# Kernel tuning notes

Hardware: AMD Instinct MI355X
Metric: run time of the kernel (lower is better)

## Reference

```python
import jax, jax.numpy as jnp
import numpy as np

ALPHA = 0.2  # LeakyReLU slope in GAT
OUT_SLOPE = 0.01  # default nn.LeakyyReLU slope for self.out
B, E, IN_DIM, HID, HEADS = 4, 2048, 32, 18, 3
DH = HID // HEADS  # per-head out dim = 6


def _leaky(x, slope):
    return jnp.where(x > 0, x, slope * x)


def _gat_head(x, adj, W, a):
    # x: [B,E,in], W: [in,dh], a: [2*dh,1]
    h = jnp.einsum('bei,id->bed', x, W)                      # [B,E,dh]
    d = h.shape[-1]
    # score[b,i,j] = leakyrelu(a . concat(h_i, h_j)) = leakyrelu(h_i.a1 + h_j.a2)
    e1 = jnp.einsum('bed,d->be', h, a[:d, 0])
    e2 = jnp.einsum('bed,d->be', h, a[d:, 0])
    score = _leaky(e1[:, :, None] + e2[:, None, :], ALPHA)   # [B,E,E]
    scores = jnp.where(adj == 1.0, score, 0.0)
    logits = jnp.where(adj > 0.0, scores, -30.0)
    att = jax.nn.softmax(logits, axis=2)                     # softmax over j
    # h_prime[b,j,d] = sum_i att[b,i,j] * h[b,i,d]  (torch sums over dim=1)
    h_prime = jnp.einsum('bij,bid->bjd', att, h)
    return jax.nn.elu(h_prime)  # concat=True -> elu


def _gat_multihead(x, adj, Ws, As):
    # Ws: [H,in,dh], As: [H,2*dh,1]
    outs = jax.vmap(lambda W, a: _gat_head(x, adj, W, a))(Ws, As)  # [H,B,E,dh]
    H, b, e, d = outs.shape
    return jnp.moveaxis(outs, 0, 2).reshape(b, e, H * d)  # concat heads last-dim


def _gcn(x, adj2d, W, b):
    return adj2d @ (x @ W) + b


def setup_inputs() -> dict:
    key = jax.random.key(0)
    ks = jax.random.split(key, 16)
    node_input = jax.random.normal(ks[0], (B, E, IN_DIM), jnp.float32)
    uv_filed = jax.random.normal(ks[1], (B, E, IN_DIM), jnp.float32)
    adj = jax.random.randint(ks[2], (B, E, E), 0, 2).astype(jnp.float32)
    s = 0.1
    Wt1 = jax.random.normal(ks[3], (HEADS, IN_DIM, DH), jnp.float32) * s
    at1 = jax.random.normal(ks[4], (HEADS, 2 * DH, 1), jnp.float32) * s
    Wt2 = jax.random.normal(ks[5], (HEADS, IN_DIM, DH), jnp.float32) * s
    at2 = jax.random.normal(ks[6], (HEADS, 2 * DH, 1), jnp.float32) * s
    Wg1 = jax.random.normal(ks[7], (HID, 16), jnp.float32) * s
    bg1 = jnp.zeros((16,), jnp.float32)
    Wg2 = jax.random.normal(ks[8], (16, 2), jnp.float32) * s
    bg2 = jnp.zeros((2,), jnp.float32)
    Wo1 = jax.random.normal(ks[9], (HID, 16), jnp.float32) * s
    bo1 = jnp.zeros((16,), jnp.float32)
    Wo2 = jax.random.normal(ks[10], (16, 2), jnp.float32) * s
    bo2 = jnp.zeros((2,), jnp.float32)
    return dict(node_input=node_input, uv_filed=uv_filed, adj=adj,
                Wt1=Wt1, at1=at1, Wt2=Wt2, at2=at2,
                Wg1=Wg1, bg1=bg1, Wg2=Wg2, bg2=bg2,
                Wo1=Wo1, bo1=bo1, Wo2=Wo2, bo2=bo2)


def reference(node_input, uv_filed, adj, Wt1, at1, Wt2, at2,
              Wg1, bg1, Wg2, bg2, Wo1, bo1, Wo2, bo2):
    h = _gat_multihead(node_input, adj, Wt1, at1)  # [B,E,18]
    o = _gat_multihead(uv_filed, adj, Wt2, at2)    # [B,E,18]
    a0 = adj[0]
    Y = jax.nn.relu(_gcn(h[0], a0, Wg1, bg1))
    O = jax.nn.relu(_gcn(o[0], a0, Wo1, bo1))
    Y = _gcn(Y, a0, Wg2, bg2)
    O = _gcn(O, a0, Wo2, bo2)
    return (jax.nn.log_softmax(Y, axis=1), _leaky(O, OUT_SLOPE))
```

## Files before the change

### kernel.cpp

```cpp
#include <hip/hip_runtime.h>
#include <hip/hip_bf16.h>


__global__ __launch_bounds__(256) void k01(
    const float* __restrict__ adj0, unsigned int* __restrict__ bm,
    const float* __restrict__ node, const float* __restrict__ uv,
    const float* __restrict__ Wt1, const float* __restrict__ at1,
    const float* __restrict__ Wt2, const float* __restrict__ at2,
    float* __restrict__ hcol, float4* __restrict__ pk1q, float* __restrict__ pack2) {
  int b = blockIdx.x;
  if (b < 512) {
    int lane = threadIdx.x & 63, w = threadIdx.x >> 6;
    int row = b * 4 + w;
    const float* arow = adj0 + (size_t)row * 2048;
#pragma unroll 4
    for (int it = 0; it < 32; ++it) {
      float v = arow[it * 64 + lane];
      unsigned long long mask = __ballot(v == 1.0f);
      if (lane == 0) bm[row * 64 + it * 2] = (unsigned int)mask;
      else if (lane == 32) bm[row * 64 + it * 2 + 1] = (unsigned int)(mask >> 32);
    }
    return;
  }
  __shared__ float sW[192];
  __shared__ float sA[12];
  int fb = b - 512;
  int g = fb / 24;
  int h = (fb / 8) % 3;
  int e = (fb % 8) * 256 + threadIdx.x;
  const float* W = (g ? Wt2 : Wt1) + h * 192;
  const float* A = (g ? at2 : at1) + h * 12;
  const float* x = (g ? uv : node) + e * 32;
  if (threadIdx.x < 192) sW[threadIdx.x] = W[threadIdx.x];
  if (threadIdx.x < 12) sA[threadIdx.x] = A[threadIdx.x];
  __syncthreads();
  float xv[32];
#pragma unroll
  for (int i = 0; i < 32; ++i) xv[i] = x[i];
  float hv[6];
#pragma unroll
  for (int d = 0; d < 6; ++d) hv[d] = 0.f;
#pragma unroll
  for (int i = 0; i < 32; ++i)
#pragma unroll
    for (int d = 0; d < 6; ++d) hv[d] += xv[i] * sW[i * 6 + d];
  float e1 = 0.f, e2 = 0.f;
#pragma unroll
  for (int d = 0; d < 6; ++d) {
    e1 += hv[d] * sA[d];
    e2 += hv[d] * sA[6 + d];
  }
  int c = g * 3 + h;
#pragma unroll
  for (int d = 0; d < 6; ++d) hcol[(c * 6 + d) * 2048 + e] = hv[d];
  pk1q[c * 2048 + e] = make_float4(e1, __expf(e1), __expf(0.2f * e1), 0.f);
  pack2[c * 2048 + e] = e2;
  pack2[(6 + c) * 2048 + e] = __expf(e2);
  pack2[(12 + c) * 2048 + e] = __expf(0.2f * e2);
}

__global__ __launch_bounds__(384) void k2_rowsum_hs(
    const unsigned int* __restrict__ bm, const float4* __restrict__ pk1q,
    const float* __restrict__ pack2, const float* __restrict__ hcol,
    float* __restrict__ hs8) {
  int tid = threadIdx.x;
  int c = tid >> 6, lane = tid & 63;
  int i0 = blockIdx.x * 4;
  const float4* p2_4 = (const float4*)pack2;
  float e1r[4], p1r[4], q1r[4], sum[4];
#pragma unroll
  for (int r = 0; r < 4; ++r) {
    float4 pq = pk1q[c * 2048 + i0 + r];
    e1r[r] = pq.x; p1r[r] = pq.y; q1r[r] = pq.z;
    sum[r] = 0.f;
  }
  int sh = (lane & 7) * 4;
#pragma unroll
  for (int it = 0; it < 8; ++it) {
    int j4 = it * 64 + lane;
    float4 e2 = p2_4[c * 512 + j4];
    float4 p2 = p2_4[(6 + c) * 512 + j4];
    float4 q2 = p2_4[(12 + c) * 512 + j4];
    int wbase = it * 8 + (lane >> 3);
    float abx, aby, abz, abw;
#pragma unroll
    for (int r = 0; r < 4; ++r) {
      unsigned int wd = bm[(i0 + r) * 64 + wbase] >> sh;
      { float e = e1r[r] + e2.x; bool p = e > 0.f;
        abx = (p ? p1r[r] : q1r[r]) * (p ? p2.x : q2.x); }
      { float e = e1r[r] + e2.y; bool p = e > 0.f;
        aby = (p ? p1r[r] : q1r[r]) * (p ? p2.y : q2.y); }
      { float e = e1r[r] + e2.z; bool p = e > 0.f;
        abz = (p ? p1r[r] : q1r[r]) * (p ? p2.z : q2.z); }
      { float e = e1r[r] + e2.w; bool p = e > 0.f;
        abw = (p ? p1r[r] : q1r[r]) * (p ? p2.w : q2.w); }
      float s = ((wd & 1u) ? abx : 0.f) + ((wd & 2u) ? aby : 0.f) +
                ((wd & 4u) ? abz : 0.f) + ((wd & 8u) ? abw : 0.f);
      sum[r] += s;
    }
  }
#pragma unroll
  for (int r = 0; r < 4; ++r) {
#pragma unroll
    for (int off = 32; off > 0; off >>= 1) sum[r] += __shfl_down(sum[r], off);
  }
  float s0 = __shfl(sum[0], 0), s1 = __shfl(sum[1], 0);
  float s2 = __shfl(sum[2], 0), s3 = __shfl(sum[3], 0);
  if (lane < 32) {
    int r = lane >> 3, d = lane & 7;
    float sv = (r == 0) ? s0 : (r == 1) ? s1 : (r == 2) ? s2 : s3;
    float v = 0.f;
    if (d < 6) v = hcol[(c * 6 + d) * 2048 + i0 + r] * (1.0f / sv);
    hs8[((size_t)c * 2048 + i0 + r) * 8 + d] = v;
  }
}

__global__ __launch_bounds__(384) void k3_hprime(
    const unsigned int* __restrict__ bm, const float4* __restrict__ pk1q,
    const float* __restrict__ pack2, const float4* __restrict__ hs8,
    float* __restrict__ hp_part) {
  int tid = threadIdx.x;
  int c6 = tid >> 6, jl = tid & 63;
  int j0 = blockIdx.x * 128;
  int i0 = blockIdx.y * 64;
  int jA = j0 + jl, jB = jA + 64;
  float e2A = pack2[c6 * 2048 + jA];
  float p2A = pack2[(6 + c6) * 2048 + jA];
  float q2A = pack2[(12 + c6) * 2048 + jA];
  float e2B = pack2[c6 * 2048 + jB];
  float p2B = pack2[(6 + c6) * 2048 + jB];
  float q2B = pack2[(12 + c6) * 2048 + jB];
  float aA0 = 0.f, aA1 = 0.f, aA2 = 0.f, aA3 = 0.f, aA4 = 0.f, aA5 = 0.f;
  float aB0 = 0.f, aB1 = 0.f, aB2 = 0.f, aB3 = 0.f, aB4 = 0.f, aB5 = 0.f;
  int hi = jl >> 5;
  int shj = jl & 31;
  const float4* pk1 = pk1q + c6 * 2048;
  const float4* hs = hs8 + (size_t)c6 * 2048 * 2;
  const unsigned int* bmA = bm + (size_t)i0 * 64 + (j0 >> 5) + hi;
#pragma unroll 4
  for (int ii = 0; ii < 64; ++ii) {
    int irow = i0 + ii;
    float4 pk = pk1[irow];
    float4 h0 = hs[irow * 2];
    float4 h1 = hs[irow * 2 + 1];
    unsigned int wdA = bmA[ii * 64];
    unsigned int wdB = bmA[ii * 64 + 2];
    {
      float e = pk.x + e2A; bool p = e > 0.f;
      float ab = (p ? pk.y : pk.z) * (p ? p2A : q2A);
      float w = ((wdA >> shj) & 1u) ? ab : 0.f;
      aA0 += w * h0.x; aA1 += w * h0.y; aA2 += w * h0.z;
      aA3 += w * h0.w; aA4 += w * h1.x; aA5 += w * h1.y;
    }
    {
      float e = pk.x + e2B; bool p = e > 0.f;
      float ab = (p ? pk.y : pk.z) * (p ? p2B : q2B);
      float w = ((wdB >> shj) & 1u) ? ab : 0.f;
      aB0 += w * h0.x; aB1 += w * h0.y; aB2 += w * h0.z;
      aB3 += w * h0.w; aB4 += w * h1.x; aB5 += w * h1.y;
    }
  }
  float* hp = hp_part + (size_t)blockIdx.y * 73728;
  int kb = c6 * 6;
  hp[(kb + 0) * 2048 + jA] = aA0;
  hp[(kb + 1) * 2048 + jA] = aA1;
  hp[(kb + 2) * 2048 + jA] = aA2;
  hp[(kb + 3) * 2048 + jA] = aA3;
  hp[(kb + 4) * 2048 + jA] = aA4;
  hp[(kb + 5) * 2048 + jA] = aA5;
  hp[(kb + 0) * 2048 + jB] = aB0;
  hp[(kb + 1) * 2048 + jB] = aB1;
  hp[(kb + 2) * 2048 + jB] = aB2;
  hp[(kb + 3) * 2048 + jB] = aB3;
  hp[(kb + 4) * 2048 + jB] = aB4;
  hp[(kb + 5) * 2048 + jB] = aB5;
}

__global__ __launch_bounds__(256) void k4_T(
    const float* __restrict__ hp_part, const float* __restrict__ Wg1,
    const float* __restrict__ Wo1, float* __restrict__ T) {
  __shared__ float sHP[8 * 37];
  __shared__ float sWg[288], sWo[288];
  int tid = threadIdx.x;
  int j0 = blockIdx.x * 8;
  for (int idx = tid; idx < 288; idx += 256) {
    sWg[idx] = Wg1[idx];
    sWo[idx] = Wo1[idx];
  }
  for (int idx = tid; idx < 288; idx += 256) {
    int r = idx >> 3, jl = idx & 7;
    float s = 0.f;
#pragma unroll
    for (int sp = 0; sp < 32; ++sp)
      s += hp_part[(size_t)sp * 73728 + r * 2048 + j0 + jl];
    sHP[jl * 37 + r] = s > 0.f ? s : __expf(s) - 1.f;
  }
  __syncthreads();
  int jl = tid >> 5, col = tid & 31;
  int gat = col >> 4, cc = col & 15;
  const float* Wp = gat ? sWo : sWg;
  float a = 0.f;
#pragma unroll
  for (int r = 0; r < 18; ++r)
    a += sHP[jl * 37 + gat * 18 + r] * Wp[r * 16 + cc];
  T[(j0 + jl) * 32 + col] = a;
}

__global__ __launch_bounds__(256) void k5_gcn1(
    const unsigned int* __restrict__ bm, const float* __restrict__ T,
    float* __restrict__ Craw_part) {
  __shared__ unsigned int sM[64 * 4];
  __shared__ float4 sT4[128 * 8];
  const float4* T4 = (const float4*)T;
  int tid = threadIdx.x;
  int rl = tid & 31, cg = tid >> 5;
  int i0 = blockIdx.x * 64;
  int k0 = blockIdx.y * 128;
  sM[tid] = bm[(size_t)(i0 + (tid >> 2)) * 64 + (k0 >> 5) + (tid & 3)];
  for (int idx = tid; idx < 1024; idx += 256) sT4[idx] = T4[k0 * 8 + idx];
  __syncthreads();
  float a0x = 0.f, a0y = 0.f, a0z = 0.f, a0w = 0.f;
  float a1x = 0.f, a1y = 0.f, a1z = 0.f, a1w = 0.f;
#pragma unroll
  for (int wi = 0; wi < 4; ++wi) {
    unsigned int wA = sM[rl * 4 + wi];
    unsigned int wB = sM[(rl + 32) * 4 + wi];
#pragma unroll 16
    for (int kb = 0; kb < 32; ++kb) {
      float4 t = sT4[(wi * 32 + kb) * 8 + cg];
      float mA = (float)((wA >> kb) & 1u);
      float mB = (float)((wB >> kb) & 1u);
      a0x += mA * t.x; a0y += mA * t.y; a0z += mA * t.z; a0w += mA * t.w;
      a1x += mB * t.x; a1y += mB * t.y; a1z += mB * t.z; a1w += mB * t.w;
    }
  }
  float* base = Craw_part + (size_t)blockIdx.y * 65536;
  *(float4*)&base[(i0 + rl) * 32 + cg * 4] = make_float4(a0x, a0y, a0z, a0w);
  *(float4*)&base[(i0 + rl + 32) * 32 + cg * 4] = make_float4(a1x, a1y, a1z, a1w);
}

__global__ __launch_bounds__(256) void k6_T2(
    const float* __restrict__ Craw_part, const float* __restrict__ bg1,
    const float* __restrict__ Wg2, const float* __restrict__ bo1,
    const float* __restrict__ Wo2, float* __restrict__ T2) {
  int tid = threadIdx.x;
  int wave = tid >> 6, lane = tid & 63;
  int j = blockIdx.x * 8 + wave * 2 + (lane >> 5);
  int cl = lane & 31;
  int gat = cl >> 4, cc = cl & 15;
  float x = 0.f;
#pragma unroll
  for (int sp = 0; sp < 16; ++sp) x += Craw_part[(size_t)sp * 65536 + j * 32 + cl];
  x += gat ? bo1[cc] : bg1[cc];
  x = x > 0.f ? x : 0.f;
  float wa = gat ? Wo2[cc * 2 + 0] : Wg2[cc * 2 + 0];
  float wb = gat ? Wo2[cc * 2 + 1] : Wg2[cc * 2 + 1];
  float pa = x * wa, pb = x * wb;
#pragma unroll
  for (int m = 8; m > 0; m >>= 1) {
    pa += __shfl_xor(pa, m);
    pb += __shfl_xor(pb, m);
  }
  if (cc == 0) {
    T2[j * 4 + gat * 2 + 0] = pa;
    T2[j * 4 + gat * 2 + 1] = pb;
  }
}

__global__ __launch_bounds__(256) void k7_final(
    const unsigned int* __restrict__ bm, const float* __restrict__ T2,
    const float* __restrict__ bg2, const float* __restrict__ bo2,
    float* __restrict__ out) {
  int tid = threadIdx.x;
  int lane = tid & 63, w = tid >> 6;
  int r = blockIdx.x * 4 + w;
  const float4* T24 = (const float4*)T2;
  float4 acc = make_float4(0.f, 0.f, 0.f, 0.f);
  int sh = lane & 31;
#pragma unroll 8
  for (int it = 0; it < 32; ++it) {
    int k = it * 64 + lane;
    unsigned int wd = bm[r * 64 + it * 2 + (lane >> 5)];
    float m = (float)((wd >> sh) & 1u);
    float4 t = T24[k];
    acc.x += m * t.x;
    acc.y += m * t.y;
    acc.z += m * t.z;
    acc.w += m * t.w;
  }
#pragma unroll
  for (int off = 32; off > 0; off >>= 1) {
    acc.x += __shfl_down(acc.x, off);
    acc.y += __shfl_down(acc.y, off);
    acc.z += __shfl_down(acc.z, off);
    acc.w += __shfl_down(acc.w, off);
  }
  if (lane == 0) {
    float y0 = acc.x + bg2[0], y1 = acc.y + bg2[1];
    float m = fmaxf(y0, y1);
    float ls = m + logf(__expf(y0 - m) + __expf(y1 - m));
    out[r * 2 + 0] = y0 - ls;
    out[r * 2 + 1] = y1 - ls;
    float o0 = acc.z + bo2[0], o1 = acc.w + bo2[1];
    out[4096 + r * 2 + 0] = o0 > 0.f ? o0 : 0.01f * o0;
    out[4096 + r * 2 + 1] = o1 > 0.f ? o1 : 0.01f * o1;
  }
}

extern "C" void kernel_launch(void* const* d_in, const int* in_sizes, int n_in,
                              void* d_out, int out_size, void* d_ws, size_t ws_size,
                              hipStream_t stream) {
  const float* node = (const float*)d_in[0];
  const float* uv = (const float*)d_in[1];
  const float* adj = (const float*)d_in[2];
  const float* Wt1 = (const float*)d_in[3];
  const float* at1 = (const float*)d_in[4];
  const float* Wt2 = (const float*)d_in[5];
  const float* at2 = (const float*)d_in[6];
  const float* Wg1 = (const float*)d_in[7];
  const float* bg1 = (const float*)d_in[8];
  const float* Wg2 = (const float*)d_in[9];
  const float* bg2 = (const float*)d_in[10];
  const float* Wo1 = (const float*)d_in[11];
  const float* bo1 = (const float*)d_in[12];
  const float* Wo2 = (const float*)d_in[13];
  const float* bo2 = (const float*)d_in[14];
  float* ws = (float*)d_ws;
  float* hcol = ws;
  float* pack2 = ws + 73728;
  float4* pk1q = (float4*)(ws + 110592);
  float* hs8 = ws + 159744;
  float* T = ws + 258048;
  float* T2 = ws + 323584;
  unsigned int* bm = (unsigned int*)(ws + 331776);
  float* hp_part = ws + 462848;
  float* Craw_part = ws + 2822144;
  float* out = (float*)d_out;

  k01<<<560, 256, 0, stream>>>(adj, bm, node, uv, Wt1, at1, Wt2, at2,
                               hcol, pk1q, pack2);
  k2_rowsum_hs<<<512, 384, 0, stream>>>(bm, pk1q, pack2, hcol, hs8);
  k3_hprime<<<dim3(16, 32), 384, 0, stream>>>(bm, pk1q, pack2, (const float4*)hs8, hp_part);
  k4_T<<<256, 256, 0, stream>>>(hp_part, Wg1, Wo1, T);
  k5_gcn1<<<dim3(32, 16), 256, 0, stream>>>(bm, T, Craw_part);
  k6_T2<<<256, 256, 0, stream>>>(Craw_part, bg1, Wg2, bo1, Wo2, T2);
  k7_final<<<512, 256, 0, stream>>>(bm, T2, bg2, bo2, out);
}
```

Baseline: 200.9 us.

## Fuse seven kernels into one cooperative persistent kernel with grid syncs

Replaces the seven separate kernel launches with a single cooperative kernel of 256 blocks that runs each stage as a phase separated by grid-wide syncs. Work is redistributed so each block handles larger chunks, with fewer split partials in the attention and GCN stages. The aim is to remove per-launch overhead and inter-kernel gaps. The cost is fewer blocks per phase, which lowers parallelism, plus the latency of the grid barriers. A fallback multi-kernel path is kept in case the cooperative launch fails.

```diff
diff --git a/kernel.cpp b/kernel.cpp
--- a/kernel.cpp
+++ b/kernel.cpp
@@ -1,75 +1,80 @@
 #include <hip/hip_runtime.h>
+#include <hip/hip_cooperative_groups.h>
 #include <hip/hip_bf16.h>
 
-
-__global__ __launch_bounds__(256) void k01(
-    const float* __restrict__ adj0, unsigned int* __restrict__ bm,
+namespace cg = cooperative_groups;
+
+
+#define NB 256
+#define NT 384
+
+__device__ __forceinline__ void phase0(
+    int b, int tid, const float* __restrict__ adj0, unsigned int* __restrict__ bm,
     const float* __restrict__ node, const float* __restrict__ uv,
     const float* __restrict__ Wt1, const float* __restrict__ at1,
     const float* __restrict__ Wt2, const float* __restrict__ at2,
     float* __restrict__ hcol, float4* __restrict__ pk1q, float* __restrict__ pack2) {
-  int b = blockIdx.x;
-  if (b < 512) {
-    int lane = threadIdx.x & 63, w = threadIdx.x >> 6;
-    int row = b * 4 + w;
-    const float* arow = adj0 + (size_t)row * 2048;
+  int w6 = tid >> 6, lane = tid & 63;
+  if (w6 < 4) {
+#pragma unroll
+    for (int rep = 0; rep < 2; ++rep) {
+      int row = b * 8 + rep * 4 + w6;
+      const float* arow = adj0 + (size_t)row * 2048;
 #pragma unroll 4
-    for (int it = 0; it < 32; ++it) {
-      float v = arow[it * 64 + lane];
-      unsigned long long mask = __ballot(v == 1.0f);
-      if (lane == 0) bm[row * 64 + it * 2] = (unsigned int)mask;
-      else if (lane == 32) bm[row * 64 + it * 2 + 1] = (unsigned int)(mask >> 32);
-    }
-    return;
-  }
-  __shared__ float sW[192];
-  __shared__ float sA[12];
-  int fb = b - 512;
-  int g = fb / 24;
-  int h = (fb / 8) % 3;
-  int e = (fb % 8) * 256 + threadIdx.x;
-  const float* W = (g ? Wt2 : Wt1) + h * 192;
-  const float* A = (g ? at2 : at1) + h * 12;
-  const float* x = (g ? uv : node) + e * 32;
-  if (threadIdx.x < 192) sW[threadIdx.x] = W[threadIdx.x];
-  if (threadIdx.x < 12) sA[threadIdx.x] = A[threadIdx.x];
-  __syncthreads();
-  float xv[32];
-#pragma unroll
-  for (int i = 0; i < 32; ++i) xv[i] = x[i];
-  float hv[6];
-#pragma unroll
-  for (int d = 0; d < 6; ++d) hv[d] = 0.f;
-#pragma unroll
-  for (int i = 0; i < 32; ++i)
-#pragma unroll
-    for (int d = 0; d < 6; ++d) hv[d] += xv[i] * sW[i * 6 + d];
-  float e1 = 0.f, e2 = 0.f;
-#pragma unroll
-  for (int d = 0; d < 6; ++d) {
-    e1 += hv[d] * sA[d];
-    e2 += hv[d] * sA[6 + d];
-  }
-  int c = g * 3 + h;
-#pragma unroll
-  for (int d = 0; d < 6; ++d) hcol[(c * 6 + d) * 2048 + e] = hv[d];
-  pk1q[c * 2048 + e] = make_float4(e1, __expf(e1), __expf(0.2f * e1), 0.f);
-  pack2[c * 2048 + e] = e2;
-  pack2[(6 + c) * 2048 + e] = __expf(e2);
-  pack2[(12 + c) * 2048 + e] = __expf(0.2f * e2);
-}
-
-__global__ __launch_bounds__(384) void k2_rowsum_hs(
-    const unsigned int* __restrict__ bm, const float4* __restrict__ pk1q,
-    const float* __restrict__ pack2, const float* __restrict__ hcol,
-    float* __restrict__ hs8) {
-  int tid = threadIdx.x;
+      for (int it = 0; it < 32; ++it) {
+        float v = arow[it * 64 + lane];
+        unsigned long long mask = __ballot(v == 1.0f);
+        if (lane == 0) bm[row * 64 + it * 2] = (unsigned int)mask;
+        else if (lane == 32) bm[row * 64 + it * 2 + 1] = (unsigned int)(mask >> 32);
+      }
+    }
+  }
+  if (tid >= 256 && tid < 272) {
+    int unit = b * 16 + (tid - 256);
+    int g = unit >> 11;
+    int e = unit & 2047;
+    const float* W = g ? Wt2 : Wt1;
+    const float* A = g ? at2 : at1;
+    const float* x = (g ? uv : node) + e * 32;
+    float xv[32];
+#pragma unroll
+    for (int i = 0; i < 32; ++i) xv[i] = x[i];
+#pragma unroll
+    for (int h = 0; h < 3; ++h) {
+      float hv[6];
+#pragma unroll
+      for (int d = 0; d < 6; ++d) hv[d] = 0.f;
+#pragma unroll
+      for (int i = 0; i < 32; ++i)
+#pragma unroll
+        for (int d = 0; d < 6; ++d) hv[d] += xv[i] * W[h * 192 + i * 6 + d];
+      float e1 = 0.f, e2 = 0.f;
+#pragma unroll
+      for (int d = 0; d < 6; ++d) {
+        e1 += hv[d] * A[h * 12 + d];
+        e2 += hv[d] * A[h * 12 + 6 + d];
+      }
+      int c = g * 3 + h;
+#pragma unroll
+      for (int d = 0; d < 6; ++d) hcol[(c * 6 + d) * 2048 + e] = hv[d];
+      pk1q[c * 2048 + e] = make_float4(e1, __expf(e1), __expf(0.2f * e1), 0.f);
+      pack2[c * 2048 + e] = e2;
+      pack2[(6 + c) * 2048 + e] = __expf(e2);
+      pack2[(12 + c) * 2048 + e] = __expf(0.2f * e2);
+    }
+  }
+}
+
+__device__ __forceinline__ void phase1(
+    int b, int tid, const unsigned int* __restrict__ bm,
+    const float4* __restrict__ pk1q, const float* __restrict__ pack2,
+    const float* __restrict__ hcol, float* __restrict__ hs8) {
   int c = tid >> 6, lane = tid & 63;
-  int i0 = blockIdx.x * 4;
+  int i0 = b * 8;
   const float4* p2_4 = (const float4*)pack2;
-  float e1r[4], p1r[4], q1r[4], sum[4];
-#pragma unroll
-  for (int r = 0; r < 4; ++r) {
+  float e1r[8], p1r[8], q1r[8], sum[8];
+#pragma unroll
+  for (int r = 0; r < 8; ++r) {
     float4 pq = pk1q[c * 2048 + i0 + r];
     e1r[r] = pq.x; p1r[r] = pq.y; q1r[r] = pq.z;
     sum[r] = 0.f;
@@ -84,7 +89,7 @@
     int wbase = it * 8 + (lane >> 3);
     float abx, aby, abz, abw;
 #pragma unroll
-    for (int r = 0; r < 4; ++r) {
+    for (int r = 0; r < 8; ++r) {
       unsigned int wd = bm[(i0 + r) * 64 + wbase] >> sh;
       { float e = e1r[r] + e2.x; bool p = e > 0.f;
         abx = (p ? p1r[r] : q1r[r]) * (p ? p2.x : q2.x); }
@@ -100,29 +105,28 @@
     }
   }
 #pragma unroll
-  for (int r = 0; r < 4; ++r) {
+  for (int r = 0; r < 8; ++r) {
 #pragma unroll
     for (int off = 32; off > 0; off >>= 1) sum[r] += __shfl_down(sum[r], off);
   }
   float s0 = __shfl(sum[0], 0), s1 = __shfl(sum[1], 0);
   float s2 = __shfl(sum[2], 0), s3 = __shfl(sum[3], 0);
-  if (lane < 32) {
-    int r = lane >> 3, d = lane & 7;
-    float sv = (r == 0) ? s0 : (r == 1) ? s1 : (r == 2) ? s2 : s3;
-    float v = 0.f;
-    if (d < 6) v = hcol[(c * 6 + d) * 2048 + i0 + r] * (1.0f / sv);
-    hs8[((size_t)c * 2048 + i0 + r) * 8 + d] = v;
-  }
-}
-
-__global__ __launch_bounds__(384) void k3_hprime(
-    const unsigned int* __restrict__ bm, const float4* __restrict__ pk1q,
-    const float* __restrict__ pack2, const float4* __restrict__ hs8,
-    float* __restrict__ hp_part) {
-  int tid = threadIdx.x;
+  float s4 = __shfl(sum[4], 0), s5 = __shfl(sum[5], 0);
+  float s6 = __shfl(sum[6], 0), s7 = __shfl(sum[7], 0);
+  int r = lane >> 3, d = lane & 7;
+  float sv = r < 4 ? (r < 2 ? (r == 0 ? s0 : s1) : (r == 2 ? s2 : s3))
+                   : (r < 6 ? (r == 4 ? s4 : s5) : (r == 6 ? s6 : s7));
+  float v = (d < 6) ? hcol[(c * 6 + d) * 2048 + i0 + r] * (1.0f / sv) : 0.f;
+  hs8[((size_t)c * 2048 + i0 + r) * 8 + d] = v;
+}
+
+__device__ __forceinline__ void phase2(
+    int b, int tid, const unsigned int* __restrict__ bm,
+    const float4* __restrict__ pk1q, const float* __restrict__ pack2,
+    const float4* __restrict__ hs8_4, float* __restrict__ hp_part) {
   int c6 = tid >> 6, jl = tid & 63;
-  int j0 = blockIdx.x * 128;
-  int i0 = blockIdx.y * 64;
+  int j0 = (b & 15) * 128;
+  int i0 = (b >> 4) * 128;
   int jA = j0 + jl, jB = jA + 64;
   float e2A = pack2[c6 * 2048 + jA];
   float p2A = pack2[(6 + c6) * 2048 + jA];
@@ -135,10 +139,10 @@
   int hi = jl >> 5;
   int shj = jl & 31;
   const float4* pk1 = pk1q + c6 * 2048;
-  const float4* hs = hs8 + (size_t)c6 * 2048 * 2;
+  const float4* hs = hs8_4 + (size_t)c6 * 2048 * 2;
   const unsigned int* bmA = bm + (size_t)i0 * 64 + (j0 >> 5) + hi;
 #pragma unroll 4
-  for (int ii = 0; ii < 64; ++ii) {
+  for (int ii = 0; ii < 128; ++ii) {
     int irow = i0 + ii;
     float4 pk = pk1[irow];
     float4 h0 = hs[irow * 2];
@@ -148,19 +152,19 @@
     {
       float e = pk.x + e2A; bool p = e > 0.f;
       float ab = (p ? pk.y : pk.z) * (p ? p2A : q2A);
-      float w = ((wdA >> shj) & 1u) ? ab : 0.f;
-      aA0 += w * h0.x; aA1 += w * h0.y; aA2 += w * h0.z;
-      aA3 += w * h0.w; aA4 += w * h1.x; aA5 += w * h1.y;
+      float wg = ((wdA >> shj) & 1u) ? ab : 0.f;
+      aA0 += wg * h0.x; aA1 += wg * h0.y; aA2 += wg * h0.z;
+      aA3 += wg * h0.w; aA4 += wg * h1.x; aA5 += wg * h1.y;
     }
     {
       float e = pk.x + e2B; bool p = e > 0.f;
       float ab = (p ? pk.y : pk.z) * (p ? p2B : q2B);
-      float w = ((wdB >> shj) & 1u) ? ab : 0.f;
-      aB0 += w * h0.x; aB1 += w * h0.y; aB2 += w * h0.z;
-      aB3 += w * h0.w; aB4 += w * h1.x; aB5 += w * h1.y;
-    }
-  }
-  float* hp = hp_part + (size_t)blockIdx.y * 73728;
+      float wg = ((wdB >> shj) & 1u) ? ab : 0.f;
+      aB0 += wg * h0.x; aB1 += wg * h0.y; aB2 += wg * h0.z;
+      aB3 += wg * h0.w; aB4 += wg * h1.x; aB5 += wg * h1.y;
+    }
+  }
+  float* hp = hp_part + (size_t)(b >> 4) * 73728;
   int kb = c6 * 6;
   hp[(kb + 0) * 2048 + jA] = aA0;
   hp[(kb + 1) * 2048 + jA] = aA1;
@@ -176,86 +180,100 @@
   hp[(kb + 5) * 2048 + jB] = aB5;
 }
 
-__global__ __launch_bounds__(256) void k4_T(
-    const float* __restrict__ hp_part, const float* __restrict__ Wg1,
-    const float* __restrict__ Wo1, float* __restrict__ T) {
-  __shared__ float sHP[8 * 37];
-  __shared__ float sWg[288], sWo[288];
-  int tid = threadIdx.x;
-  int j0 = blockIdx.x * 8;
-  for (int idx = tid; idx < 288; idx += 256) {
+__device__ __forceinline__ void phase3(
+    int b, int tid, char* smem, const float* __restrict__ hp_part,
+    const float* __restrict__ Wg1, const float* __restrict__ Wo1,
+    float* __restrict__ T) {
+  float* sHP = (float*)smem;
+  float* sWg = sHP + 296;
+  float* sWo = sWg + 288;
+  int j0 = b * 8;
+  for (int idx = tid; idx < 288; idx += NT) {
     sWg[idx] = Wg1[idx];
     sWo[idx] = Wo1[idx];
   }
-  for (int idx = tid; idx < 288; idx += 256) {
+  for (int idx = tid; idx < 288; idx += NT) {
     int r = idx >> 3, jl = idx & 7;
     float s = 0.f;
 #pragma unroll
-    for (int sp = 0; sp < 32; ++sp)
+    for (int sp = 0; sp < 16; ++sp)
       s += hp_part[(size_t)sp * 73728 + r * 2048 + j0 + jl];
     sHP[jl * 37 + r] = s > 0.f ? s : __expf(s) - 1.f;
   }
   __syncthreads();
-  int jl = tid >> 5, col = tid & 31;
-  int gat = col >> 4, cc = col & 15;
-  const float* Wp = gat ? sWo : sWg;
-  float a = 0.f;
-#pragma unroll
-  for (int r = 0; r < 18; ++r)
-    a += sHP[jl * 37 + gat * 18 + r] * Wp[r * 16 + cc];
-  T[(j0 + jl) * 32 + col] = a;
-}
-
-__global__ __launch_bounds__(256) void k5_gcn1(
-    const unsigned int* __restrict__ bm, const float* __restrict__ T,
-    float* __restrict__ Craw_part) {
-  __shared__ unsigned int sM[64 * 4];
-  __shared__ float4 sT4[128 * 8];
+  if (tid < 256) {
+    int jl = tid >> 5, col = tid & 31;
+    int gat = col >> 4, cc = col & 15;
+    const float* Wp = gat ? sWo : sWg;
+    float a = 0.f;
+#pragma unroll
+    for (int r = 0; r < 18; ++r)
+      a += sHP[jl * 37 + gat * 18 + r] * Wp[r * 16 + cc];
+    T[(j0 + jl) * 32 + col] = a;
+  }
+  __syncthreads();
+}
+
+__device__ __forceinline__ void phase4(
+    int b, int tid, char* smem, const unsigned int* __restrict__ bm,
+    const float* __restrict__ T, float* __restrict__ Craw_part) {
+  unsigned int* sM = (unsigned int*)smem;
+  float4* sT4 = (float4*)(smem + 2048);
   const float4* T4 = (const float4*)T;
-  int tid = threadIdx.x;
-  int rl = tid & 31, cg = tid >> 5;
-  int i0 = blockIdx.x * 64;
-  int k0 = blockIdx.y * 128;
-  sM[tid] = bm[(size_t)(i0 + (tid >> 2)) * 64 + (k0 >> 5) + (tid & 3)];
-  for (int idx = tid; idx < 1024; idx += 256) sT4[idx] = T4[k0 * 8 + idx];
-  __syncthreads();
+  int i0 = (b & 31) * 64;
+  int k0 = (b >> 5) * 256;
+  for (int idx = tid; idx < 512; idx += NT)
+    sM[idx] = bm[(size_t)(i0 + (idx >> 3)) * 64 + (k0 >> 5) + (idx & 7)];
+  int rl = tid & 31, cg2 = tid >> 5;
   float a0x = 0.f, a0y = 0.f, a0z = 0.f, a0w = 0.f;
   float a1x = 0.f, a1y = 0.f, a1z = 0.f, a1w = 0.f;
 #pragma unroll
-  for (int wi = 0; wi < 4; ++wi) {
-    unsigned int wA = sM[rl * 4 + wi];
-    unsigned int wB = sM[(rl + 32) * 4 + wi];
+  for (int st = 0; st < 2; ++st) {
+    __syncthreads();
+    for (int idx = tid; idx < 1024; idx += NT)
+      sT4[idx] = T4[(k0 + st * 128) * 8 + idx];
+    __syncthreads();
+    if (tid < 256) {
+#pragma unroll
+      for (int wi = 0; wi < 4; ++wi) {
+        unsigned int wA = sM[rl * 8 + st * 4 + wi];
+        unsigned int wB = sM[(rl + 32) * 8 + st * 4 + wi];
 #pragma unroll 16
-    for (int kb = 0; kb < 32; ++kb) {
-      float4 t = sT4[(wi * 32 + kb) * 8 + cg];
-      float mA = (float)((wA >> kb) & 1u);
-      float mB = (float)((wB >> kb) & 1u);
-      a0x += mA * t.x; a0y += mA * t.y; a0z += mA * t.z; a0w += mA * t.w;
-      a1x += mB * t.x; a1y += mB * t.y; a1z += mB * t.z; a1w += mB * t.w;
-    }
-  }
-  float* base = Craw_part + (size_t)blockIdx.y * 65536;
-  *(float4*)&base[(i0 + rl) * 32 + cg * 4] = make_float4(a0x, a0y, a0z, a0w);
-  *(float4*)&base[(i0 + rl + 32) * 32 + cg * 4] = make_float4(a1x, a1y, a1z, a1w);
-}
-
-__global__ __launch_bounds__(256) void k6_T2(
-    const float* __restrict__ Craw_part, const float* __restrict__ bg1,
-    const float* __restrict__ Wg2, const float* __restrict__ bo1,
-    const float* __restrict__ Wo2, float* __restrict__ T2) {
-  int tid = threadIdx.x;
-  int wave = tid >> 6, lane = tid & 63;
-  int j = blockIdx.x * 8 + wave * 2 + (lane >> 5);
-  int cl = lane & 31;
+        for (int kb = 0; kb < 32; ++kb) {
+          float4 t = sT4[(wi * 32 + kb) * 8 + cg2];
+          float mA = (float)((wA >> kb) & 1u);
+          float mB = (float)((wB >> kb) & 1u);
+          a0x += mA * t.x; a0y += mA * t.y; a0z += mA * t.z; a0w += mA * t.w;
+          a1x += mB * t.x; a1y += mB * t.y; a1z += mB * t.z; a1w += mB * t.w;
+        }
+      }
+    }
+  }
+  if (tid < 256) {
+    float* base = Craw_part + (size_t)(b >> 5) * 65536;
+    *(float4*)&base[(i0 + rl) * 32 + cg2 * 4] = make_float4(a0x, a0y, a0z, a0w);
+    *(float4*)&base[(i0 + rl + 32) * 32 + cg2 * 4] = make_float4(a1x, a1y, a1z, a1w);
+  }
+  __syncthreads();
+}
+
+__device__ __forceinline__ void phase5(
+    int b, int tid, const float* __restrict__ Craw_part,
+    const float* __restrict__ bg1, const float* __restrict__ Wg2,
+    const float* __restrict__ bo1, const float* __restrict__ Wo2,
+    float* __restrict__ T2) {
+  if (tid >= 256) return;
+  int j = b * 8 + (tid >> 5);
+  int cl = tid & 31;
   int gat = cl >> 4, cc = cl & 15;
   float x = 0.f;
 #pragma unroll
-  for (int sp = 0; sp < 16; ++sp) x += Craw_part[(size_t)sp * 65536 + j * 32 + cl];
+  for (int sp = 0; sp < 8; ++sp)
+    x += Craw_part[(size_t)sp * 65536 + j * 32 + cl];
   x += gat ? bo1[cc] : bg1[cc];
   x = x > 0.f ? x : 0.f;
-  float wa = gat ? Wo2[cc * 2 + 0] : Wg2[cc * 2 + 0];
-  float wb = gat ? Wo2[cc * 2 + 1] : Wg2[cc * 2 + 1];
-  float pa = x * wa, pb = x * wb;
+  float pa = x * (gat ? Wo2[cc * 2 + 0] : Wg2[cc * 2 + 0]);
+  float pb = x * (gat ? Wo2[cc * 2 + 1] : Wg2[cc * 2 + 1]);
 #pragma unroll
   for (int m = 8; m > 0; m >>= 1) {
     pa += __shfl_xor(pa, m);
@@ -267,44 +285,110 @@
   }
 }
 
-__global__ __launch_bounds__(256) void k7_final(
-    const unsigned int* __restrict__ bm, const float* __restrict__ T2,
-    const float* __restrict__ bg2, const float* __restrict__ bo2,
-    float* __restrict__ out) {
-  int tid = threadIdx.x;
-  int lane = tid & 63, w = tid >> 6;
-  int r = blockIdx.x * 4 + w;
+__device__ __forceinline__ void phase6(
+    int b, int tid, const unsigned int* __restrict__ bm,
+    const float* __restrict__ T2, const float* __restrict__ bg2,
+    const float* __restrict__ bo2, float* __restrict__ out) {
+  int w6 = tid >> 6, lane = tid & 63;
+  if (w6 >= 4) return;
   const float4* T24 = (const float4*)T2;
-  float4 acc = make_float4(0.f, 0.f, 0.f, 0.f);
   int sh = lane & 31;
+#pragma unroll
+  for (int rep = 0; rep < 2; ++rep) {
+    int r = b * 8 + rep * 4 + w6;
+    float4 acc = make_float4(0.f, 0.f, 0.f, 0.f);
 #pragma unroll 8
-  for (int it = 0; it < 32; ++it) {
-    int k = it * 64 + lane;
-    unsigned int wd = bm[r * 64 + it * 2 + (lane >> 5)];
-    float m = (float)((wd >> sh) & 1u);
-    float4 t = T24[k];
-    acc.x += m * t.x;
-    acc.y += m * t.y;
-    acc.z += m * t.z;
-    acc.w += m * t.w;
-  }
-#pragma unroll
-  for (int off = 32; off > 0; off >>= 1) {
-    acc.x += __shfl_down(acc.x, off);
-    acc.y += __shfl_down(acc.y, off);
-    acc.z += __shfl_down(acc.z, off);
-    acc.w += __shfl_down(acc.w, off);
-  }
-  if (lane == 0) {
-    float y0 = acc.x + bg2[0], y1 = acc.y + bg2[1];
-    float m = fmaxf(y0, y1);
-    float ls = m + logf(__expf(y0 - m) + __expf(y1 - m));
-    out[r * 2 + 0] = y0 - ls;
-    out[r * 2 + 1] = y1 - ls;
-    float o0 = acc.z + bo2[0], o1 = acc.w + bo2[1];
-    out[4096 + r * 2 + 0] = o0 > 0.f ? o0 : 0.01f * o0;
-    out[4096 + r * 2 + 1] = o1 > 0.f ? o1 : 0.01f * o1;
-  }
+    for (int it = 0; it < 32; ++it) {
+      int k = it * 64 + lane;
+      unsigned int wd = bm[r * 64 + it * 2 + (lane >> 5)];
+      float m = (float)((wd >> sh) & 1u);
+      float4 t = T24[k];
+      acc.x += m * t.x;
+      acc.y += m * t.y;
+      acc.z += m * t.z;
+      acc.w += m * t.w;
+    }
+#pragma unroll
+    for (int off = 32; off > 0; off >>= 1) {
+      acc.x += __shfl_down(acc.x, off);
+      acc.y += __shfl_down(acc.y, off);
+      acc.z += __shfl_down(acc.z, off);
+      acc.w += __shfl_down(acc.w, off);
+    }
+    if (lane == 0) {
+      float y0 = acc.x + bg2[0], y1 = acc.y + bg2[1];
+      float m = fmaxf(y0, y1);
+      float ls = m + logf(__expf(y0 - m) + __expf(y1 - m));
+      out[r * 2 + 0] = y0 - ls;
+      out[r * 2 + 1] = y1 - ls;
+      float o0 = acc.z + bo2[0], o1 = acc.w + bo2[1];
+      out[4096 + r * 2 + 0] = o0 > 0.f ? o0 : 0.01f * o0;
+      out[4096 + r * 2 + 1] = o1 > 0.f ? o1 : 0.01f * o1;
+    }
+  }
+}
+
+__global__ __launch_bounds__(NT, 2) void gat_gcn_mono(
+    const float* adj0, unsigned int* bm, const float* node, const float* uv,
+    const float* Wt1, const float* at1, const float* Wt2, const float* at2,
+    float* hcol, float4* pk1q, float* pack2, float* hs8, float* hp_part,
+    const float* Wg1, const float* Wo1, float* T, float* Craw_part,
+    const float* bg1, const float* Wg2, const float* bo1, const float* Wo2,
+    float* T2, const float* bg2, const float* bo2, float* out) {
+  cg::grid_group grid = cg::this_grid();
+  __shared__ __align__(16) char smem[18432];
+  int b = blockIdx.x, tid = threadIdx.x;
+  phase0(b, tid, adj0, bm, node, uv, Wt1, at1, Wt2, at2, hcol, pk1q, pack2);
+  grid.sync();
+  phase1(b, tid, bm, pk1q, pack2, hcol, hs8);
+  grid.sync();
+  phase2(b, tid, bm, pk1q, pack2, (const float4*)hs8, hp_part);
+  grid.sync();
+  phase3(b, tid, smem, hp_part, Wg1, Wo1, T);
+  grid.sync();
+  phase4(b, tid, smem, bm, T, Craw_part);
+  grid.sync();
+  phase5(b, tid, Craw_part, bg1, Wg2, bo1, Wo2, T2);
+  grid.sync();
+  phase6(b, tid, bm, T2, bg2, bo2, out);
+}
+
+__global__ __launch_bounds__(NT, 2) void f0(
+    const float* adj0, unsigned int* bm, const float* node, const float* uv,
+    const float* Wt1, const float* at1, const float* Wt2, const float* at2,
+    float* hcol, float4* pk1q, float* pack2) {
+  phase0(blockIdx.x, threadIdx.x, adj0, bm, node, uv, Wt1, at1, Wt2, at2,
+         hcol, pk1q, pack2);
+}
+__global__ __launch_bounds__(NT, 2) void f1(
+    const unsigned int* bm, const float4* pk1q, const float* pack2,
+    const float* hcol, float* hs8) {
+  phase1(blockIdx.x, threadIdx.x, bm, pk1q, pack2, hcol, hs8);
+}
+__global__ __launch_bounds__(NT, 2) void f2(
+    const unsigned int* bm, const float4* pk1q, const float* pack2,
+    const float4* hs8_4, float* hp_part) {
+  phase2(blockIdx.x, threadIdx.x, bm, pk1q, pack2, hs8_4, hp_part);
+}
+__global__ __launch_bounds__(NT, 2) void f3(
+    const float* hp_part, const float* Wg1, const float* Wo1, float* T) {
+  __shared__ __align__(16) char smem[3584];
+  phase3(blockIdx.x, threadIdx.x, smem, hp_part, Wg1, Wo1, T);
+}
+__global__ __launch_bounds__(NT, 2) void f4(
+    const unsigned int* bm, const float* T, float* Craw_part) {
+  __shared__ __align__(16) char smem[18432];
+  phase4(blockIdx.x, threadIdx.x, smem, bm, T, Craw_part);
+}
+__global__ __launch_bounds__(NT, 2) void f5(
+    const float* Craw_part, const float* bg1, const float* Wg2,
+    const float* bo1, const float* Wo2, float* T2) {
+  phase5(blockIdx.x, threadIdx.x, Craw_part, bg1, Wg2, bo1, Wo2, T2);
+}
+__global__ __launch_bounds__(NT, 2) void f6(
+    const unsigned int* bm, const float* T2, const float* bg2,
+    const float* bo2, float* out) {
+  phase6(blockIdx.x, threadIdx.x, bm, T2, bg2, bo2, out);
 }
 
 extern "C" void kernel_launch(void* const* d_in, const int* in_sizes, int n_in,
@@ -334,15 +418,26 @@
   float* T2 = ws + 323584;
   unsigned int* bm = (unsigned int*)(ws + 331776);
   float* hp_part = ws + 462848;
-  float* Craw_part = ws + 2822144;
+  float* Craw_part = ws + 1642496;
   float* out = (float*)d_out;
 
-  k01<<<560, 256, 0, stream>>>(adj, bm, node, uv, Wt1, at1, Wt2, at2,
-                               hcol, pk1q, pack2);
-  k2_rowsum_hs<<<512, 384, 0, stream>>>(bm, pk1q, pack2, hcol, hs8);
-  k3_hprime<<<dim3(16, 32), 384, 0, stream>>>(bm, pk1q, pack2, (const float4*)hs8, hp_part);
-  k4_T<<<256, 256, 0, stream>>>(hp_part, Wg1, Wo1, T);
-  k5_gcn1<<<dim3(32, 16), 256, 0, stream>>>(bm, T, Craw_part);
-  k6_T2<<<256, 256, 0, stream>>>(Craw_part, bg1, Wg2, bo1, Wo2, T2);
-  k7_final<<<512, 256, 0, stream>>>(bm, T2, bg2, bo2, out);
-}
+  void* args[] = {
+      (void*)&adj, (void*)&bm, (void*)&node, (void*)&uv,
+      (void*)&Wt1, (void*)&at1, (void*)&Wt2, (void*)&at2,
+      (void*)&hcol, (void*)&pk1q, (void*)&pack2, (void*)&hs8,
+      (void*)&hp_part, (void*)&Wg1, (void*)&Wo1, (void*)&T,
+      (void*)&Craw_part, (void*)&bg1, (void*)&Wg2, (void*)&bo1,
+      (void*)&Wo2, (void*)&T2, (void*)&bg2, (void*)&bo2, (void*)&out};
+  hipError_t err = hipLaunchCooperativeKernel(
+      (const void*)gat_gcn_mono, dim3(NB), dim3(NT), args, 0, stream);
+  if (err != hipSuccess) {
+    f0<<<NB, NT, 0, stream>>>(adj, bm, node, uv, Wt1, at1, Wt2, at2,
+                              hcol, pk1q, pack2);
+    f1<<<NB, NT, 0, stream>>>(bm, pk1q, pack2, hcol, hs8);
+    f2<<<NB, NT, 0, stream>>>(bm, pk1q, pack2, (const float4*)hs8, hp_part);
+    f3<<<NB, NT, 0, stream>>>(hp_part, Wg1, Wo1, T);
+    f4<<<NB, NT, 0, stream>>>(bm, T, Craw_part);
+    f5<<<NB, NT, 0, stream>>>(Craw_part, bg1, Wg2, bo1, Wo2, T2);
+    f6<<<NB, NT, 0, stream>>>(bm, T2, bg2, bo2, out);
+  }
+}
```

New measurement: 383.9 us. 91.1% more time.
